# Kernel optimization log

Measured on AMD Instinct MI355X. Metric: run time of the kernel, lower is better.

## Reference

```python
import jax, jax.numpy as jnp
import numpy as np

N, L, M, NNZ, P, G, H = 4096, 64, 256, 100000, 3, 1, 8
D = M // H  # head_dim = 32


def setup_inputs() -> dict:
    key = jax.random.key(0)
    ks = jax.random.split(key, 8)
    return {
        "sparse_values": jax.random.normal(ks[0], (NNZ, M), jnp.float32),
        "linear_index": jax.random.randint(ks[1], (N, L), 0, NNZ, jnp.int32),
        "is_specified": jax.random.randint(ks[2], (N, L), 0, 2, jnp.int32).astype(bool),
        "query": jax.random.normal(ks[3], (N, M), jnp.float32),
        "key_weight": jax.random.normal(ks[4], (M, M), jnp.float32) * 0.05,
        "value_weight": jax.random.normal(ks[5], (M, M), jnp.float32) * 0.05,
        "key_positions": jax.random.uniform(ks[6], (N, L, P), jnp.float32),
        "rope_freqs": jax.random.normal(ks[7], (P, G, H, D // 2), jnp.float32),
        "n_heads": H,
    }


def reference(sparse_values, linear_index, is_specified, query, key_weight,
              value_weight, key_positions, rope_freqs, n_heads):
    n, l = linear_index.shape
    m = query.shape[-1]
    h = n_heads
    d = m // h
    scale = 1.0 / np.sqrt(m)  # docstring: default scale_factor = 1/sqrt(M)

    # Gather each query's key subset; unspecified keys -> 0 (will be masked)
    safe_idx = jnp.where(is_specified, linear_index, 0)
    gathered = jnp.where(is_specified[..., None], sparse_values[safe_idx], 0.0)  # [N,L,M]

    # Key / value projections (nn.Linear convention: x @ W.T)
    k = (gathered @ key_weight.T).reshape(n, l, h, d)
    v = (gathered @ value_weight.T).reshape(n, l, h, d)

    # RoPE on keys: angles [N,L,H,D/2], summed over position dims P and freq groups G
    angles = jnp.einsum('nlp,pghd->nlhd', key_positions, rope_freqs)
    cos, sin = jnp.cos(angles), jnp.sin(angles)
    k_even, k_odd = k[..., 0::2], k[..., 1::2]
    k = jnp.stack([k_even * cos - k_odd * sin,
                   k_even * sin + k_odd * cos], axis=-1).reshape(n, l, h, d)

    # Per-query subset attention (query is pre-rotated per docstring)
    q = query.reshape(n, h, d)
    scores = jnp.einsum('nhd,nlhd->nhl', q, k) * scale
    scores = jnp.where(is_specified[:, None, :], scores, -jnp.inf)

    # Queries with all keys unspecified -> zero output (avoid NaN from all -inf)
    any_spec = is_specified.any(axis=-1)  # [N]
    attn = jax.nn.softmax(jnp.where(any_spec[:, None, None], scores, 0.0), axis=-1)
    out = jnp.einsum('nhl,nlhd->nhd', attn, v).reshape(n, m)
    out = jnp.where(any_spec[:, None], out, 0.0)
    return out, is_specified
```

## Files before the change

kernel.cpp:

```cpp
#include <hip/hip_runtime.h>
#include <math.h>

#define N_Q 4096
#define L_K 64
#define M_D 256

typedef float f32x16 __attribute__((ext_vector_type(16)));
typedef __bf16 b16x8 __attribute__((ext_vector_type(8)));
union F8 { uint4 u; unsigned short s[8]; b16x8 v; };

__device__ __forceinline__ unsigned short f2bf(float x) {
  unsigned u = __float_as_uint(x);
  return (unsigned short)((u + 0x7fffu + ((u >> 16) & 1u)) >> 16);
}

__global__ __launch_bounds__(256) void k_prep(const unsigned char* __restrict__ raw,
                                              float* __restrict__ out2,
                                              const float* __restrict__ wv,
                                              float* __restrict__ wvt,
                                              const float* __restrict__ wk,
                                              unsigned short* __restrict__ wkf,
                                              const int* __restrict__ lin,
                                              int* __restrict__ pcnt,
                                              int* __restrict__ plin,
                                              unsigned char* __restrict__ pl) {
  __shared__ int pll_s[256];
  __shared__ unsigned char pls_s[256];
  __shared__ int pc_s[4];
  const int tid = threadIdx.x, lane = tid & 63;
  pll_s[tid] = 0;
  pls_s[tid] = 0;
  int v = 0;
  for (int i = tid; i < 4096; i += 256)
    if (i & 3) v |= raw[i];
  int f = __syncthreads_or(v);
  const int gi = blockIdx.x * 256 + tid;
  bool b = f ? (raw[gi] != 0) : (((const int*)raw)[gi] != 0);
  out2[gi] = b ? 1.0f : 0.0f;
  int li = lin[gi];
  unsigned long long mask = __ballot(b);
  if (b) {
    int rank = __popcll(mask & ((1ull << lane) - 1));
    pll_s[(tid & 192) + rank] = li;
    pls_s[(tid & 192) + rank] = (unsigned char)lane;
  }
  if (lane == 0) pc_s[tid >> 6] = __popcll(mask);
  __syncthreads();
  plin[gi] = pll_s[tid];
  pl[gi] = pls_s[tid];
  if (tid < 4) pcnt[blockIdx.x * 4 + tid] = pc_s[tid];

  if (gi < 65536) {
    wvt[(gi & 255) * 256 + (gi >> 8)] = wv[gi];
    int oc = gi >> 8, k = gi & 255;
    int tt = oc >> 5, c32o = oc & 31;
    int ks = k >> 4, kg2 = (k >> 3) & 1, j = k & 7;
    wkf[(((tt * 16 + ks) << 6) + kg2 * 32 + c32o) * 8 + j] = f2bf(wk[gi]);
  }
}

#define SC_OFF  32768
#define AT_OFF  (SC_OFF + 2048)
#define LDS_SZ  (AT_OFF + 2048)

__global__ __launch_bounds__(256, 4) void k_fused7(
    const float* __restrict__ sv, const float* __restrict__ q,
    const unsigned short* __restrict__ wkf, const float* __restrict__ pos,
    const float* __restrict__ freqs, const int* __restrict__ pcnt,
    const int* __restrict__ plin, const unsigned char* __restrict__ pl,
    unsigned short* __restrict__ agg) {
  __shared__ __align__(16) char smem[LDS_SZ];
  float* sc_s   = (float*)(smem + SC_OFF);
  float* attn_s = (float*)(smem + AT_OFF);
  const int tid = threadIdx.x, lane = tid & 63, w = tid >> 6;
  const int c32 = lane & 31, kg = lane >> 5;
  const int rt = w >> 1, ch = w & 1;
  const int n = blockIdx.x;
  const int cnt = pcnt[n];

  if (cnt == 0) {
    *(uint4*)((char*)agg + (size_t)n * 4096 + tid * 16) = uint4{0, 0, 0, 0};
    return;
  }
  const int ct32 = (cnt + 31) & ~31;
  const int ntiles = ct32 >> 5;

  {
    const int r0 = tid >> 5, ii = tid & 31;
    const float* rp[8];
    #pragma unroll
    for (int pp = 0; pp < 8; ++pp) {
      const int rloc = pp * 8 + r0;
      const int pe = (rloc < cnt) ? rloc : (cnt - 1);
      rp[pp] = sv + (size_t)plin[n * 64 + pe] * 256 + ii * 8;
    }
    float4 fa[8], fb2[8];
    #pragma unroll
    for (int pp = 0; pp < 8; ++pp) {
      const int rloc = pp * 8 + r0;
      if (rloc < ct32) {
        fa[pp]  = *(const float4*)(rp[pp]);
        fb2[pp] = *(const float4*)(rp[pp] + 4);
      }
    }
    #pragma unroll
    for (int pp = 0; pp < 8; ++pp) {
      const int rloc = pp * 8 + r0;
      if (rloc < ct32) {
        F8 pk;
        pk.s[0] = f2bf(fa[pp].x); pk.s[1] = f2bf(fa[pp].y);
        pk.s[2] = f2bf(fa[pp].z); pk.s[3] = f2bf(fa[pp].w);
        pk.s[4] = f2bf(fb2[pp].x); pk.s[5] = f2bf(fb2[pp].y);
        pk.s[6] = f2bf(fb2[pp].z); pk.s[7] = f2bf(fb2[pp].w);
        *(uint4*)(smem + rloc * 512 + ((ii ^ (rloc & 31)) << 4)) = pk.u;
      }
    }
  }

  const int p = rt * 32 + c32;
  const bool pv = p < cnt;
  const int pe2 = pv ? p : (cnt - 1);
  const int l = pl[n * 64 + pe2];
  const float* lp = pos + ((size_t)n * 64 + l) * 3;
  const float pp0 = lp[0], pp1 = lp[1], pp2 = lp[2];

  __syncthreads();

  if (rt < ntiles) {
    f32x16 acc[4];
    #pragma unroll
    for (int t = 0; t < 4; ++t)
      #pragma unroll
      for (int r = 0; r < 16; ++r) acc[t][r] = 0.0f;

    const char* fbase = (const char*)wkf + ch * 65536 + lane * 16;
    F8 afc[4], afn[4];
    #pragma unroll
    for (int t = 0; t < 4; ++t) afc[t].u = *(const uint4*)(fbase + (t * 16) * 1024);

    #pragma unroll
    for (int ks = 0; ks < 16; ++ks) {
      if (ks < 15) {
        #pragma unroll
        for (int t = 0; t < 4; ++t)
          afn[t].u = *(const uint4*)(fbase + (t * 16 + ks + 1) * 1024);
      }
      F8 bf;
      bf.u = *(const uint4*)(smem + (rt * 32 + c32) * 512 + ((((ks << 1) + kg) ^ c32) << 4));
      #pragma unroll
      for (int t = 0; t < 4; ++t)
        acc[t] = __builtin_amdgcn_mfma_f32_32x32x16_bf16(afc[t].v, bf.v, acc[t], 0, 0, 0);
      #pragma unroll
      for (int t = 0; t < 4; ++t) afc[t] = afn[t];
    }

    #pragma unroll
    for (int t = 0; t < 4; ++t) {
      const int h = ch * 4 + t;
      const float* qh = q + (size_t)n * 256 + h * 32;
      const float* F = freqs + h * 16;
      float s = 0.f;
      #pragma unroll
      for (int g = 0; g < 4; ++g) {
        #pragma unroll
        for (int pr = 0; pr < 2; ++pr) {
          const int d0 = g * 8 + kg * 4 + pr * 2;
          const int jj = d0 >> 1;
          const int r = g * 4 + pr * 2;
          float ke = acc[t][r], ko = acc[t][r + 1];
          float ang = pp0 * F[jj] + pp1 * F[128 + jj] + pp2 * F[256 + jj];
          float sn = __sinf(ang), cs = __cosf(ang);
          float2 qq = *(const float2*)(qh + d0);
          s += ke * (cs * qq.x + sn * qq.y) + ko * (cs * qq.y - sn * qq.x);
        }
      }
      s += __shfl_xor(s, 32);
      if (kg == 0 && pv) sc_s[p * 8 + h] = s * 0.0625f;
    }
  }
  __syncthreads();

  #pragma unroll
  for (int uu = 0; uu < 2; ++uu) {
    const int h = w * 2 + uu;
    const bool vl = lane < cnt;
    float v = vl ? sc_s[lane * 8 + h] : -__builtin_inff();
    float mx = v;
    #pragma unroll
    for (int o = 32; o; o >>= 1) mx = fmaxf(mx, __shfl_xor(mx, o));
    float e = vl ? __expf(v - mx) : 0.f;
    float sm = e;
    #pragma unroll
    for (int o = 32; o; o >>= 1) sm += __shfl_xor(sm, o);
    if (vl) attn_s[lane * 8 + h] = e / sm;
  }
  __syncthreads();

  const int m = tid;
  float ga[8];
  #pragma unroll
  for (int h = 0; h < 8; ++h) ga[h] = 0.f;
  #pragma unroll 4
  for (int p2 = 0; p2 < cnt; ++p2) {
    unsigned short us = *(const unsigned short*)(smem + p2 * 512 +
                        ((((m >> 3) ^ (p2 & 31)) << 4) | ((m & 7) << 1)));
    float gv = __uint_as_float((unsigned)us << 16);
    const float4* ap = (const float4*)(attn_s + p2 * 8);
    float4 aA = ap[0], aB = ap[1];
    ga[0] += aA.x * gv; ga[1] += aA.y * gv; ga[2] += aA.z * gv; ga[3] += aA.w * gv;
    ga[4] += aB.x * gv; ga[5] += aB.y * gv; ga[6] += aB.z * gv; ga[7] += aB.w * gv;
  }
  #pragma unroll
  for (int h = 0; h < 8; ++h)
    agg[(size_t)n * 2048 + h * 256 + m] = f2bf(ga[h]);
}

__global__ __launch_bounds__(256) void k_out(const unsigned short* __restrict__ agg,
                                             const float* __restrict__ wvt,
                                             float* __restrict__ out) {
  __shared__ float a_s[4][8][260];
  const int tid = threadIdx.x;
  const int n0 = blockIdx.x * 4;
  #pragma unroll
  for (int it = 0; it < 4; ++it) {
    uint4 v = *(const uint4*)(agg + (size_t)(n0 + it) * 2048 + tid * 8);
    const unsigned short* sp = (const unsigned short*)&v;
    const int hh = tid >> 5, m0 = (tid & 31) * 8;
    #pragma unroll
    for (int k2 = 0; k2 < 8; ++k2)
      a_s[it][hh][m0 + k2] = __uint_as_float((unsigned)sp[k2] << 16);
  }
  __syncthreads();
  const int m = tid, h = m >> 5;
  float o0 = 0.f, o1 = 0.f, o2 = 0.f, o3 = 0.f;
  #pragma unroll 8
  for (int j = 0; j < 256; ++j) {
    float wvv = wvt[j * 256 + m];
    o0 += a_s[0][h][j] * wvv;
    o1 += a_s[1][h][j] * wvv;
    o2 += a_s[2][h][j] * wvv;
    o3 += a_s[3][h][j] * wvv;
  }
  out[(n0 + 0) * 256 + m] = o0;
  out[(n0 + 1) * 256 + m] = o1;
  out[(n0 + 2) * 256 + m] = o2;
  out[(n0 + 3) * 256 + m] = o3;
}

extern "C" void kernel_launch(void* const* d_in, const int* in_sizes, int n_in,
                              void* d_out, int out_size, void* d_ws, size_t ws_size,
                              hipStream_t stream) {
  const float* sv  = (const float*)d_in[0];
  const int* lin   = (const int*)d_in[1];
  const unsigned char* raw = (const unsigned char*)d_in[2];
  const float* q   = (const float*)d_in[3];
  const float* wk  = (const float*)d_in[4];
  const float* wv  = (const float*)d_in[5];
  const float* pos = (const float*)d_in[6];
  const float* fq  = (const float*)d_in[7];
  float* out = (float*)d_out;
  char* ws = (char*)d_ws;

  float* wvt          = (float*)ws;
  unsigned short* wkf = (unsigned short*)(ws + 262144);
  int* pcnt           = (int*)(ws + 393216);
  int* plin           = (int*)(ws + 409600);
  unsigned char* pl   = (unsigned char*)(ws + 1458176);
  unsigned short* agg = (unsigned short*)(ws + 1720320);

  k_prep  <<<1024, 256, 0, stream>>>(raw, out + N_Q * M_D, wv, wvt, wk, wkf,
                                     lin, pcnt, plin, pl);
  k_fused7<<<4096, 256, 0, stream>>>(sv, q, wkf, pos, fq, pcnt, plin, pl, agg);
  k_out   <<<1024, 256, 0, stream>>>(agg, wvt, out);
}
```

Baseline: 101.8 us.

## Process four queries per block and prefetch next query's gathered rows

The fused attention kernel now handles four queries per block in a loop. The sparse-value gather for the next query is issued into registers before the softmax and aggregation of the current one, so global latency is hidden behind compute. It also caches the rope frequencies in LDS, uses shuffles to broadcast the gather indices, and raises wave priority around the MFMA loop. In exchange the grid shrinks to a quarter of its former size, register pressure rises from the 16-float4 prefetch buffer, and the early exit for queries with zero count is removed, so fully masked queries still do the full work.

Result: slower. 363.5 us (+256.9%).

```diff
diff --git a/kernel.cpp b/kernel.cpp
--- a/kernel.cpp
+++ b/kernel.cpp
@@ -61,9 +61,10 @@
 
 #define SC_OFF  32768
 #define AT_OFF  (SC_OFF + 2048)
-#define LDS_SZ  (AT_OFF + 2048)
-
-__global__ __launch_bounds__(256, 4) void k_fused7(
+#define FR_OFF  (AT_OFF + 2048)
+#define LDS_SZ  (FR_OFF + 1536)
+
+__global__ __launch_bounds__(256, 4) void k_fused9(
     const float* __restrict__ sv, const float* __restrict__ q,
     const unsigned short* __restrict__ wkf, const float* __restrict__ pos,
     const float* __restrict__ freqs, const int* __restrict__ pcnt,
@@ -72,147 +73,186 @@
   __shared__ __align__(16) char smem[LDS_SZ];
   float* sc_s   = (float*)(smem + SC_OFF);
   float* attn_s = (float*)(smem + AT_OFF);
+  float* fr_s   = (float*)(smem + FR_OFF);
   const int tid = threadIdx.x, lane = tid & 63, w = tid >> 6;
   const int c32 = lane & 31, kg = lane >> 5;
   const int rt = w >> 1, ch = w & 1;
-  const int n = blockIdx.x;
-  const int cnt = pcnt[n];
-
-  if (cnt == 0) {
-    *(uint4*)((char*)agg + (size_t)n * 4096 + tid * 16) = uint4{0, 0, 0, 0};
-    return;
-  }
-  const int ct32 = (cnt + 31) & ~31;
-  const int ntiles = ct32 >> 5;
-
+  const int r0 = tid >> 5, ii = tid & 31;
+  const int nb = blockIdx.x * 4;
+
+  for (int i = tid; i < 384; i += 256) fr_s[i] = freqs[i];
+
+  int cnt = pcnt[nb];
   {
-    const int r0 = tid >> 5, ii = tid & 31;
+    const int mp = plin[nb * 64 + lane];
     const float* rp[8];
     #pragma unroll
     for (int pp = 0; pp < 8; ++pp) {
       const int rloc = pp * 8 + r0;
-      const int pe = (rloc < cnt) ? rloc : (cnt - 1);
-      rp[pp] = sv + (size_t)plin[n * 64 + pe] * 256 + ii * 8;
-    }
-    float4 fa[8], fb2[8];
+      const int pe = (rloc < cnt) ? rloc : 0;
+      rp[pp] = sv + (size_t)__shfl(mp, pe) * 256 + ii * 8;
+    }
+    float4 fa[16];
+    #pragma unroll
+    for (int pp = 0; pp < 8; ++pp) {
+      fa[2 * pp]     = *(const float4*)rp[pp];
+      fa[2 * pp + 1] = *(const float4*)(rp[pp] + 4);
+    }
     #pragma unroll
     for (int pp = 0; pp < 8; ++pp) {
       const int rloc = pp * 8 + r0;
-      if (rloc < ct32) {
-        fa[pp]  = *(const float4*)(rp[pp]);
-        fb2[pp] = *(const float4*)(rp[pp] + 4);
-      }
-    }
-    #pragma unroll
-    for (int pp = 0; pp < 8; ++pp) {
-      const int rloc = pp * 8 + r0;
-      if (rloc < ct32) {
-        F8 pk;
-        pk.s[0] = f2bf(fa[pp].x); pk.s[1] = f2bf(fa[pp].y);
-        pk.s[2] = f2bf(fa[pp].z); pk.s[3] = f2bf(fa[pp].w);
-        pk.s[4] = f2bf(fb2[pp].x); pk.s[5] = f2bf(fb2[pp].y);
-        pk.s[6] = f2bf(fb2[pp].z); pk.s[7] = f2bf(fb2[pp].w);
-        *(uint4*)(smem + rloc * 512 + ((ii ^ (rloc & 31)) << 4)) = pk.u;
-      }
-    }
-  }
-
-  const int p = rt * 32 + c32;
-  const bool pv = p < cnt;
-  const int pe2 = pv ? p : (cnt - 1);
-  const int l = pl[n * 64 + pe2];
-  const float* lp = pos + ((size_t)n * 64 + l) * 3;
-  const float pp0 = lp[0], pp1 = lp[1], pp2 = lp[2];
-
-  __syncthreads();
-
-  if (rt < ntiles) {
-    f32x16 acc[4];
-    #pragma unroll
-    for (int t = 0; t < 4; ++t)
-      #pragma unroll
-      for (int r = 0; r < 16; ++r) acc[t][r] = 0.0f;
-
-    const char* fbase = (const char*)wkf + ch * 65536 + lane * 16;
-    F8 afc[4], afn[4];
-    #pragma unroll
-    for (int t = 0; t < 4; ++t) afc[t].u = *(const uint4*)(fbase + (t * 16) * 1024);
-
-    #pragma unroll
-    for (int ks = 0; ks < 16; ++ks) {
-      if (ks < 15) {
+      F8 pk;
+      pk.s[0] = f2bf(fa[2 * pp].x);     pk.s[1] = f2bf(fa[2 * pp].y);
+      pk.s[2] = f2bf(fa[2 * pp].z);     pk.s[3] = f2bf(fa[2 * pp].w);
+      pk.s[4] = f2bf(fa[2 * pp + 1].x); pk.s[5] = f2bf(fa[2 * pp + 1].y);
+      pk.s[6] = f2bf(fa[2 * pp + 1].z); pk.s[7] = f2bf(fa[2 * pp + 1].w);
+      *(uint4*)(smem + rloc * 512 + ((ii ^ (rloc & 31)) << 4)) = pk.u;
+    }
+  }
+
+  #pragma unroll 1
+  for (int it = 0; it < 4; ++it) {
+    const int n = nb + it;
+    const int ntiles = (cnt + 31) >> 5;
+
+    int cnt_next = 0, mp_next = 0;
+    if (it < 3) {
+      cnt_next = pcnt[n + 1];
+      mp_next = plin[(n + 1) * 64 + lane];
+    }
+
+    __syncthreads();
+
+    const int p = rt * 32 + c32;
+    const bool pv = p < cnt;
+    const int pe2 = pv ? p : 0;
+    const int l = pl[n * 64 + pe2];
+    const float* lp = pos + ((size_t)n * 64 + l) * 3;
+    const float pp0 = lp[0], pp1 = lp[1], pp2 = lp[2];
+
+    if (rt < ntiles) {
+      f32x16 acc[4];
+      #pragma unroll
+      for (int t = 0; t < 4; ++t)
+        #pragma unroll
+        for (int r = 0; r < 16; ++r) acc[t][r] = 0.0f;
+
+      const char* fbase = (const char*)wkf + ch * 65536 + lane * 16;
+      F8 afc[4], afn[4];
+      #pragma unroll
+      for (int t = 0; t < 4; ++t) afc[t].u = *(const uint4*)(fbase + (t * 16) * 1024);
+
+      __builtin_amdgcn_s_setprio(1);
+      #pragma unroll
+      for (int ks = 0; ks < 16; ++ks) {
+        if (ks < 15) {
+          #pragma unroll
+          for (int t = 0; t < 4; ++t)
+            afn[t].u = *(const uint4*)(fbase + (t * 16 + ks + 1) * 1024);
+        }
+        F8 bf;
+        bf.u = *(const uint4*)(smem + (rt * 32 + c32) * 512 + ((((ks << 1) + kg) ^ c32) << 4));
         #pragma unroll
         for (int t = 0; t < 4; ++t)
-          afn[t].u = *(const uint4*)(fbase + (t * 16 + ks + 1) * 1024);
-      }
-      F8 bf;
-      bf.u = *(const uint4*)(smem + (rt * 32 + c32) * 512 + ((((ks << 1) + kg) ^ c32) << 4));
-      #pragma unroll
-      for (int t = 0; t < 4; ++t)
-        acc[t] = __builtin_amdgcn_mfma_f32_32x32x16_bf16(afc[t].v, bf.v, acc[t], 0, 0, 0);
-      #pragma unroll
-      for (int t = 0; t < 4; ++t) afc[t] = afn[t];
-    }
-
-    #pragma unroll
-    for (int t = 0; t < 4; ++t) {
-      const int h = ch * 4 + t;
-      const float* qh = q + (size_t)n * 256 + h * 32;
-      const float* F = freqs + h * 16;
-      float s = 0.f;
-      #pragma unroll
-      for (int g = 0; g < 4; ++g) {
+          acc[t] = __builtin_amdgcn_mfma_f32_32x32x16_bf16(afc[t].v, bf.v, acc[t], 0, 0, 0);
         #pragma unroll
-        for (int pr = 0; pr < 2; ++pr) {
-          const int d0 = g * 8 + kg * 4 + pr * 2;
-          const int jj = d0 >> 1;
-          const int r = g * 4 + pr * 2;
-          float ke = acc[t][r], ko = acc[t][r + 1];
-          float ang = pp0 * F[jj] + pp1 * F[128 + jj] + pp2 * F[256 + jj];
-          float sn = __sinf(ang), cs = __cosf(ang);
-          float2 qq = *(const float2*)(qh + d0);
-          s += ke * (cs * qq.x + sn * qq.y) + ko * (cs * qq.y - sn * qq.x);
+        for (int t = 0; t < 4; ++t) afc[t] = afn[t];
+      }
+      __builtin_amdgcn_s_setprio(0);
+
+      #pragma unroll
+      for (int t = 0; t < 4; ++t) {
+        const int h = ch * 4 + t;
+        const float* qh = q + (size_t)n * 256 + h * 32;
+        const float* F = fr_s + h * 16;
+        float s = 0.f;
+        #pragma unroll
+        for (int g = 0; g < 4; ++g) {
+          #pragma unroll
+          for (int pr = 0; pr < 2; ++pr) {
+            const int d0 = g * 8 + kg * 4 + pr * 2;
+            const int jj = d0 >> 1;
+            const int r = g * 4 + pr * 2;
+            float ke = acc[t][r], ko = acc[t][r + 1];
+            float ang = pp0 * F[jj] + pp1 * F[128 + jj] + pp2 * F[256 + jj];
+            float sn = __sinf(ang), cs = __cosf(ang);
+            float2 qq = *(const float2*)(qh + d0);
+            s += ke * (cs * qq.x + sn * qq.y) + ko * (cs * qq.y - sn * qq.x);
+          }
         }
-      }
-      s += __shfl_xor(s, 32);
-      if (kg == 0 && pv) sc_s[p * 8 + h] = s * 0.0625f;
-    }
-  }
-  __syncthreads();
-
-  #pragma unroll
-  for (int uu = 0; uu < 2; ++uu) {
-    const int h = w * 2 + uu;
-    const bool vl = lane < cnt;
-    float v = vl ? sc_s[lane * 8 + h] : -__builtin_inff();
-    float mx = v;
-    #pragma unroll
-    for (int o = 32; o; o >>= 1) mx = fmaxf(mx, __shfl_xor(mx, o));
-    float e = vl ? __expf(v - mx) : 0.f;
-    float sm = e;
-    #pragma unroll
-    for (int o = 32; o; o >>= 1) sm += __shfl_xor(sm, o);
-    if (vl) attn_s[lane * 8 + h] = e / sm;
-  }
-  __syncthreads();
-
-  const int m = tid;
-  float ga[8];
-  #pragma unroll
-  for (int h = 0; h < 8; ++h) ga[h] = 0.f;
-  #pragma unroll 4
-  for (int p2 = 0; p2 < cnt; ++p2) {
-    unsigned short us = *(const unsigned short*)(smem + p2 * 512 +
-                        ((((m >> 3) ^ (p2 & 31)) << 4) | ((m & 7) << 1)));
-    float gv = __uint_as_float((unsigned)us << 16);
-    const float4* ap = (const float4*)(attn_s + p2 * 8);
-    float4 aA = ap[0], aB = ap[1];
-    ga[0] += aA.x * gv; ga[1] += aA.y * gv; ga[2] += aA.z * gv; ga[3] += aA.w * gv;
-    ga[4] += aB.x * gv; ga[5] += aB.y * gv; ga[6] += aB.z * gv; ga[7] += aB.w * gv;
-  }
-  #pragma unroll
-  for (int h = 0; h < 8; ++h)
-    agg[(size_t)n * 2048 + h * 256 + m] = f2bf(ga[h]);
+        s += __shfl_xor(s, 32);
+        if (kg == 0 && pv) sc_s[p * 8 + h] = s * 0.0625f;
+      }
+    }
+    __syncthreads();
+
+    float4 fw[16];
+    if (it < 3) {
+      const float* rpn[8];
+      #pragma unroll
+      for (int pp = 0; pp < 8; ++pp) {
+        const int rloc = pp * 8 + r0;
+        const int pe = (rloc < cnt_next) ? rloc : 0;
+        rpn[pp] = sv + (size_t)__shfl(mp_next, pe) * 256 + ii * 8;
+      }
+      #pragma unroll
+      for (int pp = 0; pp < 8; ++pp) {
+        fw[2 * pp]     = *(const float4*)rpn[pp];
+        fw[2 * pp + 1] = *(const float4*)(rpn[pp] + 4);
+      }
+    }
+    __builtin_amdgcn_sched_barrier(0);
+
+    #pragma unroll
+    for (int uu = 0; uu < 2; ++uu) {
+      const int h = w * 2 + uu;
+      const bool vl = lane < cnt;
+      float v = vl ? sc_s[lane * 8 + h] : -__builtin_inff();
+      float mx = v;
+      #pragma unroll
+      for (int o = 32; o; o >>= 1) mx = fmaxf(mx, __shfl_xor(mx, o));
+      float e = vl ? __expf(v - mx) : 0.f;
+      float sm = e;
+      #pragma unroll
+      for (int o = 32; o; o >>= 1) sm += __shfl_xor(sm, o);
+      if (vl) attn_s[lane * 8 + h] = e / sm;
+    }
+    __syncthreads();
+
+    const int m = tid;
+    float ga[8];
+    #pragma unroll
+    for (int h = 0; h < 8; ++h) ga[h] = 0.f;
+    #pragma unroll 8
+    for (int p2 = 0; p2 < cnt; ++p2) {
+      unsigned short us = *(const unsigned short*)(smem + p2 * 512 +
+                          ((((m >> 3) ^ (p2 & 31)) << 4) | ((m & 7) << 1)));
+      float gv = __uint_as_float((unsigned)us << 16);
+      const float4* ap = (const float4*)(attn_s + p2 * 8);
+      float4 aA = ap[0], aB = ap[1];
+      ga[0] += aA.x * gv; ga[1] += aA.y * gv; ga[2] += aA.z * gv; ga[3] += aA.w * gv;
+      ga[4] += aB.x * gv; ga[5] += aB.y * gv; ga[6] += aB.z * gv; ga[7] += aB.w * gv;
+    }
+    #pragma unroll
+    for (int h = 0; h < 8; ++h)
+      agg[(size_t)n * 2048 + h * 256 + m] = f2bf(ga[h]);
+
+    __syncthreads();
+
+    if (it < 3) {
+      #pragma unroll
+      for (int pp = 0; pp < 8; ++pp) {
+        const int rloc = pp * 8 + r0;
+        F8 pk;
+        pk.s[0] = f2bf(fw[2 * pp].x);     pk.s[1] = f2bf(fw[2 * pp].y);
+        pk.s[2] = f2bf(fw[2 * pp].z);     pk.s[3] = f2bf(fw[2 * pp].w);
+        pk.s[4] = f2bf(fw[2 * pp + 1].x); pk.s[5] = f2bf(fw[2 * pp + 1].y);
+        pk.s[6] = f2bf(fw[2 * pp + 1].z); pk.s[7] = f2bf(fw[2 * pp + 1].w);
+        *(uint4*)(smem + rloc * 512 + ((ii ^ (rloc & 31)) << 4)) = pk.u;
+      }
+    }
+    cnt = cnt_next;
+  }
 }
 
 __global__ __launch_bounds__(256) void k_out(const unsigned short* __restrict__ agg,
@@ -270,6 +310,6 @@
 
   k_prep  <<<1024, 256, 0, stream>>>(raw, out + N_Q * M_D, wv, wvt, wk, wkf,
                                      lin, pcnt, plin, pl);
-  k_fused7<<<4096, 256, 0, stream>>>(sv, q, wkf, pos, fq, pcnt, plin, pl, agg);
+  k_fused9<<<1024, 256, 0, stream>>>(sv, q, wkf, pos, fq, pcnt, plin, pl, agg);
   k_out   <<<1024, 256, 0, stream>>>(agg, wvt, out);
 }
```
